# Kernel optimization log

Hardware: AMD Instinct MI355X
Metric: run time of the kernel (lower is better)

## Reference

```python
import jax, jax.numpy as jnp
import numpy as np

IMG_H, IMG_W = 800, 1344
STRIDE = 16
FH, FW = IMG_H // STRIDE, IMG_W // STRIDE  # 50, 84
C = 1024
N_PROP = 3000
K_KEEP = 512          # post-NMS proposals kept by merge_proposals
POOL = 14             # C4 ROI-align output resolution
NMS_THRESH = 0.7
NUM_CLASSES = 80


def _make_boxes(key, n):
    r = jax.random.uniform(key, (n, 4))
    cx = r[:, 0] * IMG_W
    cy = r[:, 1] * IMG_H
    w = 16.0 + r[:, 2] * 480.0
    h = 16.0 + r[:, 3] * 480.0
    x0 = jnp.clip(cx - w / 2, 0.0, IMG_W)
    y0 = jnp.clip(cy - h / 2, 0.0, IMG_H)
    x1 = jnp.clip(cx + w / 2, 0.0, IMG_W)
    y1 = jnp.clip(cy + h / 2, 0.0, IMG_H)
    return jnp.stack([x0, y0, x1, y1], axis=-1)


def setup_inputs() -> dict:
    key = jax.random.key(0)
    ks = jax.random.split(key, 14)
    feat = jax.random.normal(ks[0], (C, FH, FW), jnp.float32)
    boxes1 = _make_boxes(ks[1], N_PROP)
    boxes2 = _make_boxes(ks[2], N_PROP)
    logits1 = jax.random.normal(ks[3], (N_PROP,), jnp.float32)
    logits2 = jax.random.normal(ks[4], (N_PROP,), jnp.float32)
    levels1 = jnp.zeros((N_PROP,), jnp.int32)  # single C4 level
    levels2 = jnp.zeros((N_PROP,), jnp.int32)
    scale1 = 1.0 + 0.02 * jax.random.normal(ks[5], (C,), jnp.float32)
    bias1 = 0.02 * jax.random.normal(ks[6], (C,), jnp.float32)
    scale2 = 1.0 + 0.02 * jax.random.normal(ks[7], (C,), jnp.float32)
    bias2 = 0.02 * jax.random.normal(ks[8], (C,), jnp.float32)
    W_cls1 = 0.01 * jax.random.normal(ks[9], (C, NUM_CLASSES + 1), jnp.float32)
    b_cls1 = jnp.zeros((NUM_CLASSES + 1,), jnp.float32)
    W_box1 = 0.001 * jax.random.normal(ks[10], (C, NUM_CLASSES * 4), jnp.float32)
    b_box1 = jnp.zeros((NUM_CLASSES * 4,), jnp.float32)
    W_cls2 = 0.01 * jax.random.normal(ks[11], (C, NUM_CLASSES + 1), jnp.float32)
    b_cls2 = jnp.zeros((NUM_CLASSES + 1,), jnp.float32)
    W_box2 = 0.001 * jax.random.normal(ks[12], (C, NUM_CLASSES * 4), jnp.float32)
    b_box2 = jnp.zeros((NUM_CLASSES * 4,), jnp.float32)
    return dict(feat=feat, boxes1=boxes1, boxes2=boxes2, logits1=logits1,
                logits2=logits2, levels1=levels1, levels2=levels2,
                scale1=scale1, bias1=bias1, scale2=scale2, bias2=bias2,
                W_cls1=W_cls1, b_cls1=b_cls1, W_box1=W_box1, b_box1=b_box1,
                W_cls2=W_cls2, b_cls2=b_cls2, W_box2=W_box2, b_box2=b_box2)


def _clip_boxes(boxes):
    return jnp.stack([jnp.clip(boxes[:, 0], 0.0, IMG_W),
                      jnp.clip(boxes[:, 1], 0.0, IMG_H),
                      jnp.clip(boxes[:, 2], 0.0, IMG_W),
                      jnp.clip(boxes[:, 3], 0.0, IMG_H)], axis=-1)


def _nms(boxes, scores, k, thresh):
    """Greedy NMS; returns k kept indices (fixed-size, jit-friendly)."""
    areas = (boxes[:, 2] - boxes[:, 0]) * (boxes[:, 3] - boxes[:, 1])

    def body(i, state):
        sw, keep = state
        idx = jnp.argmax(sw)
        keep = keep.at[i].set(idx.astype(jnp.int32))
        b = boxes[idx]
        ix0 = jnp.maximum(b[0], boxes[:, 0])
        iy0 = jnp.maximum(b[1], boxes[:, 1])
        ix1 = jnp.minimum(b[2], boxes[:, 2])
        iy1 = jnp.minimum(b[3], boxes[:, 3])
        inter = jnp.maximum(ix1 - ix0, 0.0) * jnp.maximum(iy1 - iy0, 0.0)
        iou = inter / (areas[idx] + areas - inter + 1e-9)
        sw = jnp.where(iou > thresh, -jnp.inf, sw)
        sw = sw.at[idx].set(-jnp.inf)
        return sw, keep

    keep0 = jnp.zeros((k,), jnp.int32)
    _, keep = jax.lax.fori_loop(0, k, body, (scores, keep0))
    return keep


def _roi_align(feat, boxes, spatial_scale, pool):
    """ROIAlign (aligned=True, sampling_ratio=1). feat [C,H,W], boxes [R,4] -> [R,C,pool,pool]."""
    Cc, H, W = feat.shape
    b = boxes * spatial_scale - 0.5
    x0, y0, x1, y1 = b[:, 0], b[:, 1], b[:, 2], b[:, 3]
    bw = (x1 - x0) / pool
    bh = (y1 - y0) / pool
    grid = jnp.arange(pool, dtype=feat.dtype) + 0.5
    xs = x0[:, None] + grid[None, :] * bw[:, None]  # [R,P]
    ys = y0[:, None] + grid[None, :] * bh[:, None]  # [R,P]
    yf = jnp.floor(ys); xf = jnp.floor(xs)
    ly = ys - yf; lx = xs - xf
    y0c = jnp.clip(yf.astype(jnp.int32), 0, H - 1)
    y1c = jnp.clip(yf.astype(jnp.int32) + 1, 0, H - 1)
    x0c = jnp.clip(xf.astype(jnp.int32), 0, W - 1)
    x1c = jnp.clip(xf.astype(jnp.int32) + 1, 0, W - 1)

    def g(Y, X):  # gather -> [C,R,P,P]
        return feat[:, Y[:, :, None], X[:, None, :]]

    wy0 = (1.0 - ly); wy1 = ly  # [R,P]
    wx0 = (1.0 - lx); wx1 = lx
    out = (g(y0c, x0c) * (wy0[:, :, None] * wx0[:, None, :])
           + g(y0c, x1c) * (wy0[:, :, None] * wx1[:, None, :])
           + g(y1c, x0c) * (wy1[:, :, None] * wx0[:, None, :])
           + g(y1c, x1c) * (wy1[:, :, None] * wx1[:, None, :]))
    return jnp.transpose(out, (1, 0, 2, 3))  # [R,C,P,P]


def _box_head(roi_feats, scale, bias, W_cls, b_cls, W_box, b_box):
    bf = roi_feats * scale[None, :, None, None] + bias[None, :, None, None]
    x = bf.mean(axis=(2, 3))  # [R,C]
    return bf, x @ W_cls + b_cls, x @ W_box + b_box


def reference(feat, boxes1, boxes2, logits1, logits2, levels1, levels2,
              scale1, bias1, scale2, bias2,
              W_cls1, b_cls1, W_box1, b_box1,
              W_cls2, b_cls2, W_box2, b_box2):
    boxes = _clip_boxes(jnp.concatenate([boxes1, boxes2], axis=0))
    scores = jnp.concatenate([logits1, logits2], axis=0)
    levels = jnp.concatenate([levels1, levels2], axis=0)
    # batched_nms level-offset trick (all zeros for single C4 level)
    off = levels.astype(boxes.dtype)[:, None] * float(max(IMG_H, IMG_W) + 1)
    keep = _nms(boxes + off, scores, K_KEEP, NMS_THRESH)
    prop = boxes[keep]  # [K,4] merged proposals

    roi = _roi_align(feat, prop, 1.0 / STRIDE, POOL)  # [K,C,P,P]
    bf1, s1, d1 = _box_head(roi, scale1, bias1, W_cls1, b_cls1, W_box1, b_box1)
    bf2, s2, d2 = _box_head(roi, scale2, bias2, W_cls2, b_cls2, W_box2, b_box2)
    return (bf1, bf2, s1, s2, d1, prop, feat)
```

## Files before the change

### kernel.cpp

```cpp
#include <hip/hip_runtime.h>

#define FHH 50
#define FWW 84
#define HW 4200
#define NBOX 6000
#define NPAD 6144
#define KKEEP 512
#define WSTRIDE 192

typedef float f32x2 __attribute__((ext_vector_type(2)));

#define OFF_BF1  0ULL
#define OFF_BF2  102760448ULL
#define OFF_S1   205520896ULL
#define OFF_S2   205562368ULL
#define OFF_D1   205603840ULL
#define OFF_PROP 205767680ULL
#define OFF_FEAT 205769728ULL

__global__ __launch_bounds__(256) void k_transpose(const float* __restrict__ feat,
                                                   float* __restrict__ featT,
                                                   float* __restrict__ out_feat) {
  __shared__ float t[32][33];
  int hw0 = blockIdx.x * 32;
  int c0  = blockIdx.y * 32;
  int tx = threadIdx.x & 31, ty = threadIdx.x >> 5;
#pragma unroll
  for (int p = 0; p < 4; ++p) {
    int c = c0 + ty + p * 8;
    int hw = hw0 + tx;
    if (hw < HW) {
      float v = feat[(size_t)c * HW + hw];
      t[ty + p * 8][tx] = v;
      __builtin_nontemporal_store(v, &out_feat[(size_t)c * HW + hw]);
    }
  }
  __syncthreads();
#pragma unroll
  for (int p = 0; p < 4; ++p) {
    int hw = hw0 + ty + p * 8;
    int c = c0 + tx;
    if (hw < HW) featT[((size_t)hw << 10) + c] = t[tx][ty + p * 8];
  }
}

__global__ __launch_bounds__(256) void k_prep(const float4* __restrict__ boxes1,
                                              const float4* __restrict__ boxes2,
                                              const float* __restrict__ logits1,
                                              const float* __restrict__ logits2,
                                              const int* __restrict__ levels1,
                                              const int* __restrict__ levels2,
                                              float4* __restrict__ nbox,
                                              float* __restrict__ area,
                                              unsigned long long* __restrict__ keys,
                                              int* __restrict__ rank) {
  int i = blockIdx.x * 256 + threadIdx.x;
  if (i >= NPAD) return;
  if (i >= NBOX) { keys[i] = 0ULL; return; }
  rank[i] = 0;
  float4 b; float sc; int lv;
  if (i < 3000) { b = boxes1[i]; sc = logits1[i]; lv = levels1[i]; }
  else          { b = boxes2[i - 3000]; sc = logits2[i - 3000]; lv = levels2[i - 3000]; }
  float x0 = fminf(fmaxf(b.x, 0.f), 1344.f);
  float y0 = fminf(fmaxf(b.y, 0.f), 800.f);
  float x1 = fminf(fmaxf(b.z, 0.f), 1344.f);
  float y1 = fminf(fmaxf(b.w, 0.f), 800.f);
  float off = __fmul_rn((float)lv, 1345.0f);
  x0 = __fadd_rn(x0, off); y0 = __fadd_rn(y0, off);
  x1 = __fadd_rn(x1, off); y1 = __fadd_rn(y1, off);
  nbox[i] = make_float4(x0, y0, x1, y1);
  area[i] = __fmul_rn(__fsub_rn(x1, x0), __fsub_rn(y1, y0));
  unsigned u = __float_as_uint(sc);
  u = (u & 0x80000000u) ? ~u : (u | 0x80000000u);
  keys[i] = ((unsigned long long)u << 32) | (unsigned)(0xFFFFFFFFu - (unsigned)i);
}

__global__ __launch_bounds__(256) void k_rank(const unsigned long long* __restrict__ keys,
                                              int* __restrict__ rank) {
  __shared__ unsigned long long ks[1024];
  int jb = blockIdx.y;
  for (int t = threadIdx.x; t < 1024; t += 256) ks[t] = keys[jb * 1024 + t];
  __syncthreads();
  int i = blockIdx.x * 256 + threadIdx.x;
  if (i >= NBOX) return;
  unsigned long long ki = keys[i];
  int c = 0;
  for (int j = 0; j < 1024; ++j) c += (ks[j] > ki) ? 1 : 0;
  if (c) atomicAdd(&rank[i], c);
}

__global__ __launch_bounds__(256) void k_scatter(const float4* __restrict__ nbox,
                                                 const float* __restrict__ area,
                                                 const int* __restrict__ rank,
                                                 float4* __restrict__ sboxes,
                                                 float* __restrict__ sarea,
                                                 int* __restrict__ sorig) {
  int i = blockIdx.x * 256 + threadIdx.x;
  if (i >= NBOX) return;
  int r = rank[i];
  sboxes[r] = nbox[i];
  sarea[r] = area[i];
  sorig[r] = i;
}

__global__ __launch_bounds__(192) void k_mask(const float4* __restrict__ sboxes,
                                              const float* __restrict__ sarea,
                                              unsigned* __restrict__ mask) {
  int i0 = blockIdx.x * 4;
  int w = threadIdx.x;
  float4 b0 = sboxes[i0 + 0], b1 = sboxes[i0 + 1], b2 = sboxes[i0 + 2], b3 = sboxes[i0 + 3];
  float a0 = sarea[i0 + 0], a1 = sarea[i0 + 1], a2 = sarea[i0 + 2], a3 = sarea[i0 + 3];
  unsigned m0 = 0, m1 = 0, m2 = 0, m3 = 0;
  int jbase = w * 32;
  for (int bb = 0; bb < 32; ++bb) {
    int j = jbase + bb;
    if (j >= NBOX) break;
    float4 bj = sboxes[j];
    float aj = sarea[j];
#define IOU_BIT(BR, AR, MR)                                                          \
    {                                                                                \
      float ix0 = fmaxf(BR.x, bj.x), iy0 = fmaxf(BR.y, bj.y);                        \
      float ix1 = fminf(BR.z, bj.z), iy1 = fminf(BR.w, bj.w);                        \
      float iw = fmaxf(__fsub_rn(ix1, ix0), 0.f), ih = fmaxf(__fsub_rn(iy1, iy0), 0.f); \
      float inter = __fmul_rn(iw, ih);                                               \
      float den = __fadd_rn(__fsub_rn(__fadd_rn(AR, aj), inter), 1e-9f);             \
      float iou = __fdiv_rn(inter, den);                                             \
      if (iou > 0.7f) MR |= (1u << bb);                                              \
    }
    IOU_BIT(b0, a0, m0) IOU_BIT(b1, a1, m1) IOU_BIT(b2, a2, m2) IOU_BIT(b3, a3, m3)
#undef IOU_BIT
  }
  mask[(size_t)(i0 + 0) * WSTRIDE + w] = m0;
  mask[(size_t)(i0 + 1) * WSTRIDE + w] = m1;
  mask[(size_t)(i0 + 2) * WSTRIDE + w] = m2;
  mask[(size_t)(i0 + 3) * WSTRIDE + w] = m3;
}

#define SCAN_CH 64
__global__ __launch_bounds__(256) void k_scan(const unsigned* __restrict__ mask,
                                              const int* __restrict__ sorig,
                                              int* __restrict__ keep) {
  __shared__ unsigned srows[2][SCAN_CH * WSTRIDE];
  __shared__ int s_sorig[2][SCAN_CH];
  __shared__ int s_done, s_kept;
  int tid = threadIdx.x;
  if (tid == 0) { s_done = 0; s_kept = 0; }
  for (int idx = tid; idx < SCAN_CH * WSTRIDE; idx += 256) srows[0][idx] = mask[idx];
  if (tid < SCAN_CH) s_sorig[0][tid] = sorig[tid];
  __syncthreads();
  unsigned r0 = 0, r1 = 0, r2 = 0;
  int lane = tid;
  int kept = 0;
  for (int g = 0; g < 94; ++g) {
    int cur = g & 1, nxt = cur ^ 1;
    if (tid >= 64) {
      int gn = g + 1;
      if (gn < 94) {
        size_t gbase = (size_t)gn * SCAN_CH * WSTRIDE;
        for (int idx = tid - 64; idx < SCAN_CH * WSTRIDE; idx += 192) {
          size_t gi = gbase + idx;
          srows[nxt][idx] = (gi < (size_t)NBOX * WSTRIDE) ? mask[gi] : 0u;
        }
        if (tid - 64 < SCAN_CH) {
          int i2 = gn * SCAN_CH + (tid - 64);
          s_sorig[nxt][tid - 64] = (i2 < NBOX) ? sorig[i2] : 0;
        }
      }
    } else {
      int base = g * SCAN_CH;
      int nrows = min(SCAN_CH, NBOX - base);
      const unsigned* sb = srows[cur];
      unsigned p0 = sb[lane], p1 = sb[64 + lane], p2 = sb[128 + lane];
      for (int rr = 0; rr < nrows; ++rr) {
        unsigned c0v = p0, c1v = p1, c2v = p2;
        int rn = (rr + 1 < nrows) ? rr + 1 : rr;
        p0 = sb[rn * WSTRIDE + lane];
        p1 = sb[rn * WSTRIDE + 64 + lane];
        p2 = sb[rn * WSTRIDE + 128 + lane];
        int i = base + rr;
        int w = i >> 5, b = i & 31;
        int wl = w & 63, wc = w >> 6;
        unsigned rsel = (wc == 0) ? r0 : ((wc == 1) ? r1 : r2);
        unsigned rw = __shfl(rsel, wl);
        if (!((rw >> b) & 1u)) {
          r0 |= c0v; r1 |= c1v; r2 |= c2v;
          if (lane == 0) keep[kept] = s_sorig[cur][rr];
          kept++;
          if (kept >= KKEEP) break;
        }
      }
      if (lane == 0) { s_kept = kept; if (kept >= KKEEP) s_done = 1; }
    }
    __syncthreads();
    if (s_done) break;
  }
  __syncthreads();
  int fk = s_kept;
  for (int k = fk + tid; k < KKEEP; k += 256) keep[k] = 0;
}

__global__ __launch_bounds__(256) void k_prop(const int* __restrict__ keep,
                                              const float4* __restrict__ boxes1,
                                              const float4* __restrict__ boxes2,
                                              float4* __restrict__ prop) {
  int k = blockIdx.x * 256 + threadIdx.x;
  if (k >= KKEEP) return;
  int o = keep[k];
  float4 b = (o < 3000) ? boxes1[o] : boxes2[o - 3000];
  prop[k] = make_float4(fminf(fmaxf(b.x, 0.f), 1344.f),
                        fminf(fmaxf(b.y, 0.f), 800.f),
                        fminf(fmaxf(b.z, 0.f), 1344.f),
                        fminf(fmaxf(b.w, 0.f), 800.f));
}

__global__ __launch_bounds__(256) void k_bilin(const float4* __restrict__ prop,
                                               float4* __restrict__ bilinW,
                                               int4* __restrict__ bilinA) {
  int r = blockIdx.x;
  int bin = threadIdx.x;
  if (bin >= 196) return;
  float4 pb = prop[r];
  const float ss = 0.0625f;
  float x0s = pb.x * ss - 0.5f, y0s = pb.y * ss - 0.5f;
  float bw = (pb.z * ss - 0.5f - x0s) / 14.0f;
  float bh = (pb.w * ss - 0.5f - y0s) / 14.0f;
  int py = bin / 14, px = bin - py * 14;
  float xs = x0s + ((float)px + 0.5f) * bw;
  float ys = y0s + ((float)py + 0.5f) * bh;
  float xf = floorf(xs), yf = floorf(ys);
  float lx = xs - xf, ly = ys - yf;
  int ix = (int)xf, iy = (int)yf;
  int x0c = min(max(ix, 0), FWW - 1), x1c = min(max(ix + 1, 0), FWW - 1);
  int y0c = min(max(iy, 0), FHH - 1), y1c = min(max(iy + 1, 0), FHH - 1);
  float wy0 = 1.f - ly, wx0 = 1.f - lx;
  bilinW[r * 196 + bin] = make_float4(wy0 * wx0, wy0 * lx, ly * wx0, ly * lx);
  bilinA[r * 196 + bin] = make_int4((y0c * FWW + x0c) << 10, (y0c * FWW + x1c) << 10,
                                    (y1c * FWW + x0c) << 10, (y1c * FWW + x1c) << 10);
}

__global__ __launch_bounds__(256) void k_roi(const float* __restrict__ featT,
                                             const float4* __restrict__ bilinW,
                                             const int4* __restrict__ bilinA,
                                             const float* __restrict__ scale1,
                                             const float* __restrict__ bias1,
                                             const float* __restrict__ scale2,
                                             const float* __restrict__ bias2,
                                             float* __restrict__ bf1,
                                             float* __restrict__ bf2,
                                             float* __restrict__ x1w,
                                             float* __restrict__ x2w) {
  __shared__ float tile[64 * 197];
  __shared__ float part2f[4 * 64];
  __shared__ float sc1[64], bi1[64], sc2[64], bi2[64];
  int bid = blockIdx.x;
  int r = (bid & 7) + ((bid >> 7) << 3);
  int c0 = ((bid >> 3) & 15) * 64;
  int tid = threadIdx.x;
  int l16 = tid & 15, bg = tid >> 4;
  if (tid < 64) {
    sc1[tid] = scale1[c0 + tid]; bi1[tid] = bias1[c0 + tid];
    sc2[tid] = scale2[c0 + tid]; bi2[tid] = bias2[c0 + tid];
  }
  const float* fTb = featT + c0 + l16 * 4;
  const float4* bW = bilinW + r * 196;
  const int4* bA = bilinA + r * 196;
  float4 acc = make_float4(0.f, 0.f, 0.f, 0.f);

#define ROI_BODY(BB)                                                              \
  {                                                                               \
    float4 w = bW[BB]; int4 a = bA[BB];                                           \
    float4 g00 = *(const float4*)(fTb + a.x);                                     \
    float4 g01 = *(const float4*)(fTb + a.y);                                     \
    float4 g10 = *(const float4*)(fTb + a.z);                                     \
    float4 g11 = *(const float4*)(fTb + a.w);                                     \
    float vx = g00.x * w.x + g01.x * w.y + g10.x * w.z + g11.x * w.w;             \
    float vy = g00.y * w.x + g01.y * w.y + g10.y * w.z + g11.y * w.w;             \
    float vz = g00.z * w.x + g01.z * w.y + g10.z * w.z + g11.z * w.w;             \
    float vw = g00.w * w.x + g01.w * w.y + g10.w * w.z + g11.w * w.w;             \
    acc.x += vx; acc.y += vy; acc.z += vz; acc.w += vw;                           \
    int tb = l16 * 788 + (BB);                                                    \
    tile[tb] = vx; tile[tb + 197] = vy; tile[tb + 394] = vz; tile[tb + 591] = vw; \
  }

  int bb = bg;
#pragma unroll 4
  for (int i = 0; i < 12; ++i, bb += 16) ROI_BODY(bb)
  if (bg < 4) ROI_BODY(192 + bg)
#undef ROI_BODY

  acc.x += __shfl_xor(acc.x, 16); acc.y += __shfl_xor(acc.y, 16);
  acc.z += __shfl_xor(acc.z, 16); acc.w += __shfl_xor(acc.w, 16);
  acc.x += __shfl_xor(acc.x, 32); acc.y += __shfl_xor(acc.y, 32);
  acc.z += __shfl_xor(acc.z, 32); acc.w += __shfl_xor(acc.w, 32);
  if ((tid & 63) < 16) {
    int wv = tid >> 6;
    part2f[wv * 64 + l16 * 4 + 0] = acc.x;
    part2f[wv * 64 + l16 * 4 + 1] = acc.y;
    part2f[wv * 64 + l16 * 4 + 2] = acc.z;
    part2f[wv * 64 + l16 * 4 + 3] = acc.w;
  }
  __syncthreads();
  if (tid < 64) {
    float m = ((part2f[tid] + part2f[64 + tid]) + part2f[128 + tid]) + part2f[192 + tid];
    m = m / 196.0f;
    x1w[((size_t)r << 10) + c0 + tid] = m * sc1[tid] + bi1[tid];
    x2w[((size_t)r << 10) + c0 + tid] = m * sc2[tid] + bi2[tid];
  }
  size_t ob = ((size_t)((r << 10) + c0)) * 196;
  float* b1p = bf1 + ob;
  float* b2p = bf2 + ob;
  for (int it = 0; it < 25; ++it) {
    int f2 = tid + it * 256;
    if (f2 < 6272) {
      int cl = (int)((unsigned)f2 / 98u);
      int bin = (f2 - cl * 98) * 2;
      int tb = cl * 197 + bin;
      float v0 = tile[tb], v1 = tile[tb + 1];
      float s1v = sc1[cl], b1v = bi1[cl], s2v = sc2[cl], b2v = bi2[cl];
      f32x2 o1 = { v0 * s1v + b1v, v1 * s1v + b1v };
      f32x2 o2 = { v0 * s2v + b2v, v1 * s2v + b2v };
      __builtin_nontemporal_store(o1, (f32x2*)(b1p + 2 * f2));
      __builtin_nontemporal_store(o2, (f32x2*)(b2p + 2 * f2));
    }
  }
}

__global__ __launch_bounds__(256) void k_gemm(const float* __restrict__ x1,
                                              const float* __restrict__ x2,
                                              const float* __restrict__ Wc1, const float* __restrict__ bc1,
                                              const float* __restrict__ Wb1, const float* __restrict__ bb1,
                                              const float* __restrict__ Wc2, const float* __restrict__ bc2,
                                              float* __restrict__ s1, float* __restrict__ d1,
                                              float* __restrict__ s2) {
  int z = blockIdx.z;
  const float* A; const float* W; const float* bias; float* out; int N;
  if (z == 0)      { A = x1; W = Wc1; bias = bc1; out = s1; N = 81; }
  else if (z == 1) { A = x1; W = Wb1; bias = bb1; out = d1; N = 320; }
  else             { A = x2; W = Wc2; bias = bc2; out = s2; N = 81; }
  int n0 = blockIdx.y * 32;
  if (n0 >= N) return;
  int m0 = blockIdx.x * 32;
  __shared__ float As[32][34];
  __shared__ float Bs[32][34];
  int tid = threadIdx.x;
  int tx = tid & 15, ty = tid >> 4;
  float acc00 = 0, acc01 = 0, acc10 = 0, acc11 = 0;
  for (int k0 = 0; k0 < 1024; k0 += 32) {
    int mm = tid >> 3, g = tid & 7;
    float4 av = *(const float4*)(A + (size_t)(m0 + mm) * 1024 + k0 + g * 4);
    As[g * 4 + 0][mm] = av.x; As[g * 4 + 1][mm] = av.y;
    As[g * 4 + 2][mm] = av.z; As[g * 4 + 3][mm] = av.w;
    int nn = tid & 31, kh = tid >> 5;
#pragma unroll
    for (int qq = 0; qq < 4; ++qq) {
      int kk = kh + 8 * qq;
      int n = n0 + nn;
      Bs[kk][nn] = (n < N) ? W[(size_t)(k0 + kk) * N + n] : 0.f;
    }
    __syncthreads();
#pragma unroll
    for (int kk = 0; kk < 32; ++kk) {
      float2 a = *(const float2*)&As[kk][2 * ty];
      float2 b = *(const float2*)&Bs[kk][2 * tx];
      acc00 += a.x * b.x; acc01 += a.x * b.y;
      acc10 += a.y * b.x; acc11 += a.y * b.y;
    }
    __syncthreads();
  }
  int m = m0 + 2 * ty, n = n0 + 2 * tx;
  if (n < N) {
    out[(size_t)m * N + n] = acc00 + bias[n];
    out[(size_t)(m + 1) * N + n] = acc10 + bias[n];
  }
  if (n + 1 < N) {
    out[(size_t)m * N + n + 1] = acc01 + bias[n + 1];
    out[(size_t)(m + 1) * N + n + 1] = acc11 + bias[n + 1];
  }
}

extern "C" void kernel_launch(void* const* d_in, const int* in_sizes, int n_in,
                              void* d_out, int out_size, void* d_ws, size_t ws_size,
                              hipStream_t stream) {
  (void)in_sizes; (void)n_in; (void)out_size; (void)ws_size;
  const float* feat    = (const float*)d_in[0];
  const float4* boxes1 = (const float4*)d_in[1];
  const float4* boxes2 = (const float4*)d_in[2];
  const float* logits1 = (const float*)d_in[3];
  const float* logits2 = (const float*)d_in[4];
  const int* levels1   = (const int*)d_in[5];
  const int* levels2   = (const int*)d_in[6];
  const float* scale1  = (const float*)d_in[7];
  const float* bias1   = (const float*)d_in[8];
  const float* scale2  = (const float*)d_in[9];
  const float* bias2   = (const float*)d_in[10];
  const float* W_cls1  = (const float*)d_in[11];
  const float* b_cls1  = (const float*)d_in[12];
  const float* W_box1  = (const float*)d_in[13];
  const float* b_box1  = (const float*)d_in[14];
  const float* W_cls2  = (const float*)d_in[15];
  const float* b_cls2  = (const float*)d_in[16];

  float* out = (float*)d_out;
  char* w = (char*)d_ws;
  float* featT              = (float*)(w + 0);
  unsigned long long* keys  = (unsigned long long*)(w + 17203200);
  float4* nbox              = (float4*)(w + 17252352);
  float* area               = (float*)(w + 17348352);
  int* rank                 = (int*)(w + 17372352);
  float4* sboxes            = (float4*)(w + 17396352);
  float* sarea              = (float*)(w + 17492352);
  int* sorig                = (int*)(w + 17516352);
  unsigned* mask            = (unsigned*)(w + 17540352);
  int* keep                 = (int*)(w + 22148352);
  float* x1w                = (float*)(w + 22150400);
  float* x2w                = (float*)(w + 24247552);
  float4* bilinW            = (float4*)(w + 17540352);
  int4* bilinA              = (int4*)(w + 19145984);

  k_transpose<<<dim3(132, 32), 256, 0, stream>>>(feat, featT, out + OFF_FEAT);
  k_prep<<<24, 256, 0, stream>>>(boxes1, boxes2, logits1, logits2, levels1, levels2,
                                 nbox, area, keys, rank);
  k_rank<<<dim3(24, 6), 256, 0, stream>>>(keys, rank);
  k_scatter<<<24, 256, 0, stream>>>(nbox, area, rank, sboxes, sarea, sorig);
  k_mask<<<1500, 192, 0, stream>>>(sboxes, sarea, mask);
  k_scan<<<1, 256, 0, stream>>>(mask, sorig, keep);
  k_prop<<<2, 256, 0, stream>>>(keep, boxes1, boxes2, (float4*)(out + OFF_PROP));
  k_bilin<<<512, 256, 0, stream>>>((const float4*)(out + OFF_PROP), bilinW, bilinA);
  k_roi<<<8192, 256, 0, stream>>>(featT, bilinW, bilinA,
                                  scale1, bias1, scale2, bias2,
                                  out + OFF_BF1, out + OFF_BF2, x1w, x2w);
  k_gemm<<<dim3(16, 10, 3), 256, 0, stream>>>(x1w, x2w, W_cls1, b_cls1, W_box1, b_box1,
                                              W_cls2, b_cls2,
                                              out + OFF_S1, out + OFF_D1, out + OFF_S2);
}
```

Before: 483.0 us.

## Store transposed features and ROI tile in fp16, fuse prop into bilin

The transposed feature map used for ROI-align gathers is now stored as fp16, halving gather bandwidth and cache footprint. The shared-memory tile holding pooled values is also fp16, which lowers LDS use so more blocks fit per CU, and launch bounds now request 4 blocks per CU. The proposal-gather kernel is folded into the bilinear-weight kernel, removing one launch. The cost is reduced precision in the bf1/bf2 outputs and the pooled means, which may exceed the tolerance.

```diff
diff --git a/kernel.cpp b/kernel.cpp
--- a/kernel.cpp
+++ b/kernel.cpp
@@ -9,6 +9,8 @@
 #define WSTRIDE 192
 
 typedef float f32x2 __attribute__((ext_vector_type(2)));
+typedef _Float16 f16x4 __attribute__((ext_vector_type(4)));
+typedef _Float16 f16x2 __attribute__((ext_vector_type(2)));
 
 #define OFF_BF1  0ULL
 #define OFF_BF2  102760448ULL
@@ -19,7 +21,7 @@
 #define OFF_FEAT 205769728ULL
 
 __global__ __launch_bounds__(256) void k_transpose(const float* __restrict__ feat,
-                                                   float* __restrict__ featT,
+                                                   _Float16* __restrict__ featH,
                                                    float* __restrict__ out_feat) {
   __shared__ float t[32][33];
   int hw0 = blockIdx.x * 32;
@@ -40,7 +42,7 @@
   for (int p = 0; p < 4; ++p) {
     int hw = hw0 + ty + p * 8;
     int c = c0 + tx;
-    if (hw < HW) featT[((size_t)hw << 10) + c] = t[tx][ty + p * 8];
+    if (hw < HW) featH[((size_t)hw << 10) + c] = (_Float16)t[tx][ty + p * 8];
   }
 }
 
@@ -199,27 +201,28 @@
   for (int k = fk + tid; k < KKEEP; k += 256) keep[k] = 0;
 }
 
-__global__ __launch_bounds__(256) void k_prop(const int* __restrict__ keep,
-                                              const float4* __restrict__ boxes1,
-                                              const float4* __restrict__ boxes2,
-                                              float4* __restrict__ prop) {
-  int k = blockIdx.x * 256 + threadIdx.x;
-  if (k >= KKEEP) return;
-  int o = keep[k];
-  float4 b = (o < 3000) ? boxes1[o] : boxes2[o - 3000];
-  prop[k] = make_float4(fminf(fmaxf(b.x, 0.f), 1344.f),
-                        fminf(fmaxf(b.y, 0.f), 800.f),
-                        fminf(fmaxf(b.z, 0.f), 1344.f),
-                        fminf(fmaxf(b.w, 0.f), 800.f));
-}
-
-__global__ __launch_bounds__(256) void k_bilin(const float4* __restrict__ prop,
+__global__ __launch_bounds__(256) void k_bilin(const int* __restrict__ keep,
+                                               const float4* __restrict__ boxes1,
+                                               const float4* __restrict__ boxes2,
+                                               float4* __restrict__ prop,
                                                float4* __restrict__ bilinW,
                                                int4* __restrict__ bilinA) {
   int r = blockIdx.x;
+  __shared__ float4 spb;
+  if (threadIdx.x == 0) {
+    int o = keep[r];
+    float4 b = (o < 3000) ? boxes1[o] : boxes2[o - 3000];
+    float4 p = make_float4(fminf(fmaxf(b.x, 0.f), 1344.f),
+                           fminf(fmaxf(b.y, 0.f), 800.f),
+                           fminf(fmaxf(b.z, 0.f), 1344.f),
+                           fminf(fmaxf(b.w, 0.f), 800.f));
+    prop[r] = p;
+    spb = p;
+  }
+  __syncthreads();
   int bin = threadIdx.x;
   if (bin >= 196) return;
-  float4 pb = prop[r];
+  float4 pb = spb;
   const float ss = 0.0625f;
   float x0s = pb.x * ss - 0.5f, y0s = pb.y * ss - 0.5f;
   float bw = (pb.z * ss - 0.5f - x0s) / 14.0f;
@@ -238,18 +241,18 @@
                                     (y1c * FWW + x0c) << 10, (y1c * FWW + x1c) << 10);
 }
 
-__global__ __launch_bounds__(256) void k_roi(const float* __restrict__ featT,
-                                             const float4* __restrict__ bilinW,
-                                             const int4* __restrict__ bilinA,
-                                             const float* __restrict__ scale1,
-                                             const float* __restrict__ bias1,
-                                             const float* __restrict__ scale2,
-                                             const float* __restrict__ bias2,
-                                             float* __restrict__ bf1,
-                                             float* __restrict__ bf2,
-                                             float* __restrict__ x1w,
-                                             float* __restrict__ x2w) {
-  __shared__ float tile[64 * 197];
+__global__ __launch_bounds__(256, 4) void k_roi(const _Float16* __restrict__ featH,
+                                                const float4* __restrict__ bilinW,
+                                                const int4* __restrict__ bilinA,
+                                                const float* __restrict__ scale1,
+                                                const float* __restrict__ bias1,
+                                                const float* __restrict__ scale2,
+                                                const float* __restrict__ bias2,
+                                                float* __restrict__ bf1,
+                                                float* __restrict__ bf2,
+                                                float* __restrict__ x1w,
+                                                float* __restrict__ x2w) {
+  __shared__ _Float16 tile[64 * 198];
   __shared__ float part2f[4 * 64];
   __shared__ float sc1[64], bi1[64], sc2[64], bi2[64];
   int bid = blockIdx.x;
@@ -261,7 +264,7 @@
     sc1[tid] = scale1[c0 + tid]; bi1[tid] = bias1[c0 + tid];
     sc2[tid] = scale2[c0 + tid]; bi2[tid] = bias2[c0 + tid];
   }
-  const float* fTb = featT + c0 + l16 * 4;
+  const _Float16* fTb = featH + c0 + l16 * 4;
   const float4* bW = bilinW + r * 196;
   const int4* bA = bilinA + r * 196;
   float4 acc = make_float4(0.f, 0.f, 0.f, 0.f);
@@ -269,17 +272,18 @@
 #define ROI_BODY(BB)                                                              \
   {                                                                               \
     float4 w = bW[BB]; int4 a = bA[BB];                                           \
-    float4 g00 = *(const float4*)(fTb + a.x);                                     \
-    float4 g01 = *(const float4*)(fTb + a.y);                                     \
-    float4 g10 = *(const float4*)(fTb + a.z);                                     \
-    float4 g11 = *(const float4*)(fTb + a.w);                                     \
-    float vx = g00.x * w.x + g01.x * w.y + g10.x * w.z + g11.x * w.w;             \
-    float vy = g00.y * w.x + g01.y * w.y + g10.y * w.z + g11.y * w.w;             \
-    float vz = g00.z * w.x + g01.z * w.y + g10.z * w.z + g11.z * w.w;             \
-    float vw = g00.w * w.x + g01.w * w.y + g10.w * w.z + g11.w * w.w;             \
+    f16x4 g00 = *(const f16x4*)(fTb + a.x);                                       \
+    f16x4 g01 = *(const f16x4*)(fTb + a.y);                                       \
+    f16x4 g10 = *(const f16x4*)(fTb + a.z);                                       \
+    f16x4 g11 = *(const f16x4*)(fTb + a.w);                                       \
+    float vx = (float)g00.x * w.x + (float)g01.x * w.y + (float)g10.x * w.z + (float)g11.x * w.w; \
+    float vy = (float)g00.y * w.x + (float)g01.y * w.y + (float)g10.y * w.z + (float)g11.y * w.w; \
+    float vz = (float)g00.z * w.x + (float)g01.z * w.y + (float)g10.z * w.z + (float)g11.z * w.w; \
+    float vw = (float)g00.w * w.x + (float)g01.w * w.y + (float)g10.w * w.z + (float)g11.w * w.w; \
     acc.x += vx; acc.y += vy; acc.z += vz; acc.w += vw;                           \
-    int tb = l16 * 788 + (BB);                                                    \
-    tile[tb] = vx; tile[tb + 197] = vy; tile[tb + 394] = vz; tile[tb + 591] = vw; \
+    int tb = l16 * 792 + (BB);                                                    \
+    tile[tb] = (_Float16)vx; tile[tb + 198] = (_Float16)vy;                       \
+    tile[tb + 396] = (_Float16)vz; tile[tb + 594] = (_Float16)vw;                 \
   }
 
   int bb = bg;
@@ -313,9 +317,9 @@
     int f2 = tid + it * 256;
     if (f2 < 6272) {
       int cl = (int)((unsigned)f2 / 98u);
-      int bin = (f2 - cl * 98) * 2;
-      int tb = cl * 197 + bin;
-      float v0 = tile[tb], v1 = tile[tb + 1];
+      int pr = f2 - cl * 98;
+      f16x2 h = *(const f16x2*)&tile[cl * 198 + 2 * pr];
+      float v0 = (float)h.x, v1 = (float)h.y;
       float s1v = sc1[cl], b1v = bi1[cl], s2v = sc2[cl], b2v = bi2[cl];
       f32x2 o1 = { v0 * s1v + b1v, v1 * s1v + b1v };
       f32x2 o2 = { v0 * s2v + b2v, v1 * s2v + b2v };
@@ -402,7 +406,7 @@
 
   float* out = (float*)d_out;
   char* w = (char*)d_ws;
-  float* featT              = (float*)(w + 0);
+  _Float16* featH           = (_Float16*)(w + 0);
   unsigned long long* keys  = (unsigned long long*)(w + 17203200);
   float4* nbox              = (float4*)(w + 17252352);
   float* area               = (float*)(w + 17348352);
@@ -417,16 +421,16 @@
   float4* bilinW            = (float4*)(w + 17540352);
   int4* bilinA              = (int4*)(w + 19145984);
 
-  k_transpose<<<dim3(132, 32), 256, 0, stream>>>(feat, featT, out + OFF_FEAT);
+  k_transpose<<<dim3(132, 32), 256, 0, stream>>>(feat, featH, out + OFF_FEAT);
   k_prep<<<24, 256, 0, stream>>>(boxes1, boxes2, logits1, logits2, levels1, levels2,
                                  nbox, area, keys, rank);
   k_rank<<<dim3(24, 6), 256, 0, stream>>>(keys, rank);
   k_scatter<<<24, 256, 0, stream>>>(nbox, area, rank, sboxes, sarea, sorig);
   k_mask<<<1500, 192, 0, stream>>>(sboxes, sarea, mask);
   k_scan<<<1, 256, 0, stream>>>(mask, sorig, keep);
-  k_prop<<<2, 256, 0, stream>>>(keep, boxes1, boxes2, (float4*)(out + OFF_PROP));
-  k_bilin<<<512, 256, 0, stream>>>((const float4*)(out + OFF_PROP), bilinW, bilinA);
-  k_roi<<<8192, 256, 0, stream>>>(featT, bilinW, bilinA,
+  k_bilin<<<512, 256, 0, stream>>>(keep, boxes1, boxes2,
+                                   (float4*)(out + OFF_PROP), bilinW, bilinA);
+  k_roi<<<8192, 256, 0, stream>>>(featH, bilinW, bilinA,
                                   scale1, bias1, scale2, bias2,
                                   out + OFF_BF1, out + OFF_BF2, x1w, x2w);
   k_gemm<<<dim3(16, 10, 3), 256, 0, stream>>>(x1w, x2w, W_cls1, b_cls1, W_box1, b_box1,
```

After: 481.7 us. About the same (-0.3%).
